# Kernel tuning notes

Hardware: AMD Instinct MI355X
Metric: run time of the kernel (lower is better)

Reference implementation:

```python
import jax, jax.numpy as jnp
import numpy as np

B, T, C = 4, 2048, 1024
H = 16
D = C // H          # 64 head dim
CS = 128            # chunk_size (hard-coded in module)


def setup_inputs() -> dict:
    key = jax.random.key(0)
    ks = jax.random.split(key, 6)
    scale = 0.02
    x = jax.random.normal(ks[0], (B, T, C), dtype=jnp.float32)
    Wq = jax.random.normal(ks[1], (C, C), dtype=jnp.float32) * scale
    Wk = jax.random.normal(ks[2], (C, C), dtype=jnp.float32) * scale
    Wv = jax.random.normal(ks[3], (C, C), dtype=jnp.float32) * scale
    Wo = jax.random.normal(ks[4], (C, C), dtype=jnp.float32) * scale
    alpha_raw = jnp.zeros((1, H, 1, 1), dtype=jnp.float32)
    beta_raw = jnp.zeros((1, H, 1, 1), dtype=jnp.float32)
    return {"x": x, "Wq": Wq, "Wk": Wk, "Wv": Wv, "Wo": Wo,
            "alpha_raw": alpha_raw, "beta_raw": beta_raw}


def reference(x, Wq, Wk, Wv, Wo, alpha_raw, beta_raw):
    Bb, Tt, Cc = x.shape
    nc = Tt // CS
    N = Bb * H * nc  # flattened (batch, head, chunk) recurrence lanes

    # projections -> [B, H, T, D]
    def proj(W):
        return (x @ W).reshape(Bb, Tt, H, D).transpose(0, 2, 1, 3)
    q, k, v = proj(Wq), proj(Wk), proj(Wv)
    # F.normalize(k, dim=-1) with eps=1e-12
    k = k / jnp.maximum(jnp.linalg.norm(k, axis=-1, keepdims=True), 1e-12)

    alpha = jax.nn.sigmoid(alpha_raw).reshape(H) * 0.5  # [H]
    beta = jax.nn.sigmoid(beta_raw).reshape(H) * 0.5    # [H]
    a = jnp.broadcast_to(alpha[None, :, None], (Bb, H, nc)).reshape(N, 1, 1)
    b = jnp.broadcast_to(beta[None, :, None], (Bb, H, nc)).reshape(N, 1, 1)

    # chunk layout [CS, N, D] for time-major scan
    def to_scan(u):
        return u.reshape(Bb, H, nc, CS, D).reshape(N, CS, D).transpose(1, 0, 2)
    qc, kc, vc = to_scan(q), to_scan(k), to_scan(v)

    # --- per-chunk operators: A = prod(I - a k k^T), B accumulates writes ---
    def op_step(carry, kv):
        A, Bo = carry
        kt, vt = kv  # [N, D]
        Ak = jnp.einsum('nij,nj->ni', A, kt)
        A = A - a * (Ak[:, :, None] * kt[:, None, :])
        Bk = jnp.einsum('nij,nj->ni', Bo, kt)
        Bo = Bo - a * (Bk[:, :, None] * kt[:, None, :]) + b * (vt[:, :, None] * kt[:, None, :])
        return (A, Bo), None

    A0 = jnp.broadcast_to(jnp.eye(D, dtype=x.dtype), (N, D, D))
    (Aop, Bop), _ = jax.lax.scan(op_step, (A0, jnp.zeros((N, D, D), x.dtype)), (kc, vc))

    # --- inter-chunk scan: M_{i+1} = M_i A_i + B_i ---
    Aop_c = Aop.reshape(Bb, H, nc, D, D).transpose(2, 0, 1, 3, 4)
    Bop_c = Bop.reshape(Bb, H, nc, D, D).transpose(2, 0, 1, 3, 4)

    def chunk_step(M, ab):
        Ai, Bi = ab
        return jnp.einsum('bhij,bhjk->bhik', M, Ai) + Bi, M

    M_final, M_starts = jax.lax.scan(
        chunk_step, jnp.zeros((Bb, H, D, D), x.dtype), (Aop_c, Bop_c))

    # --- intra-chunk application: y_t = M_t q_t; rank-1 delta update ---
    M0 = M_starts.transpose(1, 2, 0, 3, 4).reshape(N, D, D)

    def proc_step(M, qkv):
        qt, kt, vt = qkv
        yt = jnp.einsum('nij,nj->ni', M, qt)  # == q_t @ M^T (inference path)
        Mk = jnp.einsum('nij,nj->ni', M, kt)
        M = M - a * (Mk[:, :, None] * kt[:, None, :]) + b * (vt[:, :, None] * kt[:, None, :])
        return M, yt

    _, ys = jax.lax.scan(proc_step, M0, (qc, kc, vc))  # [CS, N, D]
    y = ys.transpose(1, 0, 2).reshape(Bb, H, Tt, D)
    y = y.transpose(0, 2, 1, 3).reshape(Bb, Tt, Cc)
    y = y @ Wo  # c_proj (dropout=0 -> identity)
    return (y, M_final)
```

## Files before the change

kernel.cpp:

```cpp
#include <hip/hip_runtime.h>
#include <stdint.h>


#define DEV __device__ __forceinline__

typedef __attribute__((ext_vector_type(4))) float f32x4;
typedef __attribute__((ext_vector_type(8))) __bf16 bf16x8;
typedef __attribute__((ext_vector_type(4))) __bf16 bf16x4;

typedef const __attribute__((address_space(1))) uint32_t* gas1_t;
typedef __attribute__((address_space(3))) uint32_t* las3_t;

DEV void gload_lds16(const void* g, void* l) {
  __builtin_amdgcn_global_load_lds((gas1_t)g, (las3_t)l, 16, 0, 0);
}

DEV float sgm(float x) { return 1.f / (1.f + __expf(-x)); }

template <int CTRL>
DEV float dpp_mov(float x) {
  return __builtin_bit_cast(
      float, __builtin_amdgcn_mov_dpp(__builtin_bit_cast(int, x), CTRL, 0xF, 0xF, true));
}
DEV float row16_reduce(float x) {
  x += dpp_mov<0x121>(x);
  x += dpp_mov<0x122>(x);
  x += dpp_mov<0x124>(x);
  x += dpp_mov<0x128>(x);
  return x;
}

DEV int swzb(int row, int col, int stride) {
  return ((row * stride + col) << 1) ^ ((row & 7) << 4);
}
DEV bf16x8 ldfrag(const __bf16* B, int row, int col, int stride) {
  return *(const bf16x8*)((const char*)B + swzb(row, col, stride));
}
DEV __bf16 ldsc(const __bf16* B, int row, int col, int stride) {
  return *(const __bf16*)((const char*)B + swzb(row, col, stride));
}
DEV void stb(__bf16* B, int row, int col, int stride, __bf16 v) {
  *(__bf16*)((char*)B + swzb(row, col, stride)) = v;
}
DEV void stb4(__bf16* B, int row, int c4, int stride, bf16x4 v) {
  *(bf16x4*)((char*)B + swzb(row, c4, stride)) = v;
}
DEV int goffn(int tr) {
  int m = tr >> 1;
  return (tr & 1) ? (2 * m * m + 4 * m + 2) : (2 * m * m + 2 * m);
}
DEV int stile(int tr, int sc) { return ((tr * (tr + 1)) / 2 + sc) * 256; }

__global__ __launch_bounds__(256) void cast_f32_bf16(const float* __restrict__ in,
                                                     __bf16* __restrict__ out) {
  int idx = blockIdx.x * 256 + threadIdx.x;
  float4 v = ((const float4*)in)[idx];
  bf16x4 o;
  o[0] = (__bf16)v.x; o[1] = (__bf16)v.y; o[2] = (__bf16)v.z; o[3] = (__bf16)v.w;
  ((bf16x4*)out)[idx] = o;
}

__global__ __launch_bounds__(256) void transpose_cast(const float* __restrict__ W,
                                                      __bf16* __restrict__ Wt) {
  __shared__ float tile[32][33];
  int tx = threadIdx.x & 31, ty = threadIdx.x >> 5;
  int n0 = blockIdx.x * 32, k0 = blockIdx.y * 32;
#pragma unroll
  for (int u = 0; u < 4; ++u)
    tile[ty + u * 8][tx] = W[(size_t)(k0 + ty + u * 8) * 1024 + n0 + tx];
  __syncthreads();
#pragma unroll
  for (int u = 0; u < 4; ++u)
    Wt[(size_t)(n0 + ty + u * 8) * 1024 + k0 + tx] = (__bf16)tile[tx][ty + u * 8];
}

template <int CALLS>
DEV void stage_tile(const __bf16* __restrict__ G, __bf16* L, int t, int wid, int K) {
#pragma unroll
  for (int it = 0; it < CALLS; ++it) {
    int e = it * 512 + t;
    int row = e >> 3;
    int c0 = ((e & 7) ^ (row & 7)) << 3;
    gload_lds16(G + (size_t)row * K + c0, L + it * 4096 + wid * 512);
  }
}

__global__ __launch_bounds__(512, 2) void gemm_bt(const __bf16* __restrict__ A,
                                                  const __bf16* __restrict__ Bt,
                                                  float* __restrict__ Cf,
                                                  __bf16* __restrict__ Cb,
                                                  int mode, int NBN) {
  const int t = threadIdx.x;
  const int wid = t >> 6, lane = t & 63;
  const int fr = lane & 15, fkq = lane >> 4, fk = fkq * 8;
  const int wr = wid >> 2, wc = wid & 3;
  const int K = 1024;
  int nwg = gridDim.x, lin = blockIdx.x;
  int q = nwg >> 3;
  int id2 = (lin & 7) * q + (lin >> 3);
  int bn = id2 % NBN, bm = id2 / NBN;
  __shared__ __bf16 lA[2][16384];
  __shared__ __bf16 lB[2][16384];
  const __bf16* Ab = A + (size_t)(bm * 256) * K;
  const __bf16* Bb = Bt + (size_t)(bn * 256) * K;
  f32x4 acc[8][4];
#pragma unroll
  for (int m = 0; m < 8; ++m)
#pragma unroll
    for (int nn = 0; nn < 4; ++nn) acc[m][nn] = 0.f;
  stage_tile<4>(Ab, lA[0], t, wid, K);
  stage_tile<4>(Bb, lB[0], t, wid, K);
  for (int kt = 0; kt < 16; ++kt) {
    int cur = kt & 1;
    asm volatile("s_barrier" ::: "memory");
    if (kt < 15) {
      stage_tile<4>(Ab + (kt + 1) * 64, lA[cur ^ 1], t, wid, K);
      stage_tile<4>(Bb + (kt + 1) * 64, lB[cur ^ 1], t, wid, K);
      asm volatile("s_waitcnt vmcnt(8)" ::: "memory");
    } else {
      asm volatile("s_waitcnt vmcnt(0)" ::: "memory");
    }
    asm volatile("s_barrier" ::: "memory");
#pragma unroll
    for (int kk = 0; kk < 2; ++kk) {
      bf16x8 bg[4];
#pragma unroll
      for (int nn = 0; nn < 4; ++nn)
        bg[nn] = ldfrag(lB[cur], wc * 64 + nn * 16 + fr, kk * 32 + fk, 64);
#pragma unroll
      for (int m = 0; m < 8; ++m) {
        bf16x8 af = ldfrag(lA[cur], wr * 128 + m * 16 + fr, kk * 32 + fk, 64);
#pragma unroll
        for (int nn = 0; nn < 4; ++nn)
          acc[m][nn] =
              __builtin_amdgcn_mfma_f32_16x16x32_bf16(af, bg[nn], acc[m][nn], 0, 0, 0);
      }
    }
  }
#pragma unroll
  for (int m = 0; m < 8; ++m) {
#pragma unroll
    for (int nn = 0; nn < 4; ++nn) {
#pragma unroll
      for (int rg = 0; rg < 4; ++rg) {
        int row = bm * 256 + wr * 128 + m * 16 + fkq * 4 + rg;
        int col = bn * 256 + wc * 64 + nn * 16 + fr;
        float val = acc[m][nn][rg];
        if (mode == 0) {
          Cf[(size_t)row * 1024 + col] = val;
        } else {
          int buf = col >> 10, cc = col & 1023;
          int b = row >> 11, tk = row & 2047;
          int h = cc >> 6, d = cc & 63;
          Cb[(size_t)buf * 8388608 + (((size_t)b * 16 + h) * 2048 + tk) * 64 + d] =
              (__bf16)val;
        }
      }
    }
  }
}

__global__ __launch_bounds__(512, 6) void wy_ab(const __bf16* __restrict__ kb,
                                                const __bf16* __restrict__ vb,
                                                const float* __restrict__ ar,
                                                const float* __restrict__ br,
                                                __bf16* __restrict__ Ug,
                                                __bf16* __restrict__ Wgb,
                                                __bf16* __restrict__ ATg,
                                                __bf16* __restrict__ Bop) {
  int n = blockIdx.x, h = (n >> 4) & 15;
  float a = sgm(ar[h]) * 0.5f;
  float b = sgm(br[h]) * 0.5f;
  int t = threadIdx.x, wid = t >> 6, lane = t & 63;
  int fr = lane & 15, fkq = lane >> 4, fk = fkq * 8;
  __shared__ __attribute__((aligned(16))) char pool[51200];
  __bf16* Ks  = (__bf16*)pool;
  __bf16* MTu = (__bf16*)pool;
  __bf16* MTw = (__bf16*)(pool + 16384);
  __bf16* Sng = (__bf16*)(pool + 32768);
  __bf16* KT  = (__bf16*)(pool + 32768);
  const __bf16* kg = kb + (size_t)n * 8192;
  const __bf16* vg = vb + (size_t)n * 8192;
  bf16x8 zz;
#pragma unroll
  for (int e = 0; e < 8; ++e) zz[e] = (__bf16)0.f;
  f32x4 c0 = {0.f, 0.f, 0.f, 0.f};
  bf16x4 kreg[4];
#pragma unroll
  for (int it = 0; it < 4; ++it) {
    int u = it * 512 + t;
    int row = u >> 4, c4 = (u & 15) * 4;
    bf16x4 kh = ((const bf16x4*)kg)[u];
    float kf[4];
#pragma unroll
    for (int e = 0; e < 4; ++e) kf[e] = (float)kh[e];
    float ssq = kf[0] * kf[0] + kf[1] * kf[1] + kf[2] * kf[2] + kf[3] * kf[3];
    ssq = row16_reduce(ssq);
    float inv = 1.f / fmaxf(sqrtf(ssq), 1e-12f);
    bf16x4 kn;
#pragma unroll
    for (int e = 0; e < 4; ++e) kn[e] = (__bf16)(kf[e] * inv);
    kreg[it] = kn;
    stb4(Ks, row, c4, 64, kn);
  }
  __syncthreads();
  for (int p = wid; p < 36; p += 8) {
    int tr = 0, pp = p;
    while (pp > tr) { pp -= (tr + 1); ++tr; }
    int sc = pp;
    f32x4 acc = {0.f, 0.f, 0.f, 0.f};
#pragma unroll
    for (int ks = 0; ks < 2; ++ks)
      acc = __builtin_amdgcn_mfma_f32_16x16x32_bf16(
          ldfrag(Ks, tr * 16 + fr, ks * 32 + fk, 64),
          ldfrag(Ks, sc * 16 + fr, ks * 32 + fk, 64), acc, 0, 0, 0);
    __bf16* dst = Sng + stile(tr, sc);
#pragma unroll
    for (int rg = 0; rg < 4; ++rg) {
      int r = fkq * 4 + rg;
      float v = -a * acc[rg];
      if (tr == sc && fr >= r) v = 0.f;
      dst[r * 16 + fr] = (__bf16)v;
    }
  }
  f32x4 U[4], W[4];
#pragma unroll
  for (int ct = 0; ct < 4; ++ct) {
#pragma unroll
    for (int rg = 0; rg < 4; ++rg) {
      int row = wid * 16 + fkq * 4 + rg, col = ct * 16 + fr;
      U[ct][rg] = (float)ldsc(Ks, row, col, 64);
      W[ct][rg] = b * (float)vg[row * 64 + col];
    }
  }
  __syncthreads();
  {
    __bf16* scr  = ((__bf16*)pool) + wid * 2048;
    __bf16* tNT  = scr;
    __bf16* tN2R = scr + 256;
    __bf16* tN2T = scr + 512;
    __bf16* tN4R = scr + 768;
    __bf16* tN4T = scr + 1024;
    __bf16* tN8T = scr + 1280;
    __bf16* tPR  = scr + 1536;
    __bf16* Nd = Sng + stile(wid, wid);
    float nv[4];
#pragma unroll
    for (int rg = 0; rg < 4; ++rg) {
      nv[rg] = (float)Nd[(fkq * 4 + rg) * 16 + fr];
      tNT[fr * 16 + fkq * 4 + rg] = (__bf16)nv[rg];
    }
    asm volatile("s_waitcnt lgkmcnt(0)" ::: "memory");
    bf16x8 af = (fk < 16) ? *(const bf16x8*)(Nd + fr * 16 + fk) : zz;
    bf16x8 bop = (fk < 16) ? *(const bf16x8*)(tNT + fr * 16 + fk) : zz;
    f32x4 X = __builtin_amdgcn_mfma_f32_16x16x32_bf16(af, bop, c0, 0, 0, 0);
#pragma unroll
    for (int rg = 0; rg < 4; ++rg) {
      __bf16 v = (__bf16)X[rg];
      tN2R[(fkq * 4 + rg) * 16 + fr] = v;
      tN2T[fr * 16 + fkq * 4 + rg] = v;
    }
    asm volatile("s_waitcnt lgkmcnt(0)" ::: "memory");
    af = (fk < 16) ? *(const bf16x8*)(tN2R + fr * 16 + fk) : zz;
    bop = (fk < 16) ? *(const bf16x8*)(tN2T + fr * 16 + fk) : zz;
    X = __builtin_amdgcn_mfma_f32_16x16x32_bf16(af, bop, c0, 0, 0, 0);
#pragma unroll
    for (int rg = 0; rg < 4; ++rg) {
      __bf16 v = (__bf16)X[rg];
      tN4R[(fkq * 4 + rg) * 16 + fr] = v;
      tN4T[fr * 16 + fkq * 4 + rg] = v;
    }
    asm volatile("s_waitcnt lgkmcnt(0)" ::: "memory");
    af = (fk < 16) ? *(const bf16x8*)(tN4R + fr * 16 + fk) : zz;
    bop = (fk < 16) ? *(const bf16x8*)(tN4T + fr * 16 + fk) : zz;
    X = __builtin_amdgcn_mfma_f32_16x16x32_bf16(af, bop, c0, 0, 0, 0);
#pragma unroll
    for (int rg = 0; rg < 4; ++rg)
      tN8T[fr * 16 + fkq * 4 + rg] = (__bf16)X[rg];
    f32x4 P;
#pragma unroll
    for (int rg = 0; rg < 4; ++rg)
      P[rg] = ((fkq * 4 + rg) == fr ? 1.f : 0.f) + nv[rg];
#pragma unroll
    for (int d = 0; d < 3; ++d) {
      const __bf16* tB = (d == 0) ? tN2T : (d == 1) ? tN4T : tN8T;
#pragma unroll
      for (int rg = 0; rg < 4; ++rg)
        tPR[(fkq * 4 + rg) * 16 + fr] = (__bf16)P[rg];
      asm volatile("s_waitcnt lgkmcnt(0)" ::: "memory");
      af = (fk < 16) ? *(const bf16x8*)(tPR + fr * 16 + fk) : zz;
      bop = (fk < 16) ? *(const bf16x8*)(tB + fr * 16 + fk) : zz;
      P = __builtin_amdgcn_mfma_f32_16x16x32_bf16(af, bop, P, 0, 0, 0);
    }
#pragma unroll
    for (int rg = 0; rg < 4; ++rg)
      Nd[(fkq * 4 + rg) * 16 + fr] = (__bf16)P[rg];
  }
  __syncthreads();
  for (int bb = 0; bb < 8; ++bb) {
    if (wid == bb) {
#pragma unroll
      for (int ct = 0; ct < 4; ++ct) {
        bf16x4 uu, ww;
#pragma unroll
        for (int rg = 0; rg < 4; ++rg) {
          uu[rg] = (__bf16)U[ct][rg];
          ww[rg] = (__bf16)W[ct][rg];
        }
        stb4(MTu, ct * 16 + fr, bb * 16 + fkq * 4, 128, uu);
        stb4(MTw, ct * 16 + fr, bb * 16 + fkq * 4, 128, ww);
      }
      asm volatile("s_waitcnt lgkmcnt(0)" ::: "memory");
      const __bf16* invT = Sng + stile(bb, bb);
      bf16x8 afv = (fk < 16) ? *(const bf16x8*)(invT + fr * 16 + fk) : zz;
#pragma unroll
      for (int ct = 0; ct < 4; ++ct) {
        bf16x8 bu = (fk < 16) ? ldfrag(MTu, ct * 16 + fr, bb * 16 + fk, 128) : zz;
        bf16x8 bw = (fk < 16) ? ldfrag(MTw, ct * 16 + fr, bb * 16 + fk, 128) : zz;
        U[ct] = __builtin_amdgcn_mfma_f32_16x16x32_bf16(afv, bu, c0, 0, 0, 0);
        W[ct] = __builtin_amdgcn_mfma_f32_16x16x32_bf16(afv, bw, c0, 0, 0, 0);
      }
#pragma unroll
      for (int ct = 0; ct < 4; ++ct) {
        bf16x4 uu, ww;
#pragma unroll
        for (int rg = 0; rg < 4; ++rg) {
          uu[rg] = (__bf16)U[ct][rg];
          ww[rg] = (__bf16)W[ct][rg];
        }
        stb4(MTu, ct * 16 + fr, bb * 16 + fkq * 4, 128, uu);
        stb4(MTw, ct * 16 + fr, bb * 16 + fkq * 4, 128, ww);
      }
    }
    __syncthreads();
    if (wid > bb) {
      bf16x8 af = zz;
      if (fk < 16) af = *(const bf16x8*)(Sng + stile(wid, bb) + fr * 16 + fk);
#pragma unroll
      for (int ct = 0; ct < 4; ++ct) {
        bf16x8 bu = zz, bw = zz;
        if (fk < 16) {
          bu = ldfrag(MTu, ct * 16 + fr, bb * 16 + fk, 128);
          bw = ldfrag(MTw, ct * 16 + fr, bb * 16 + fk, 128);
        }
        U[ct] = __builtin_amdgcn_mfma_f32_16x16x32_bf16(af, bu, U[ct], 0, 0, 0);
        W[ct] = __builtin_amdgcn_mfma_f32_16x16x32_bf16(af, bw, W[ct], 0, 0, 0);
      }
    }
  }
#pragma unroll
  for (int it = 0; it < 4; ++it) {
    int u = it * 512 + t;
    int row = u >> 4, c4 = (u & 15) * 4;
#pragma unroll
    for (int e = 0; e < 4; ++e) stb(KT, c4 + e, row, 128, kreg[it][e]);
  }
  __bf16* ugo = Ug + (size_t)n * 8192;
  __bf16* wgo = Wgb + (size_t)n * 8192;
#pragma unroll
  for (int ct = 0; ct < 4; ++ct)
#pragma unroll
    for (int rg = 0; rg < 4; ++rg) {
      int row = wid * 16 + fkq * 4 + rg, col = ct * 16 + fr;
      ugo[row * 64 + col] = (__bf16)U[ct][rg];
      wgo[row * 64 + col] = (__bf16)W[ct][rg];
    }
  __syncthreads();
#pragma unroll
  for (int q = 0; q < 4; ++q) {
    int tile = wid + q * 8;
    int mat = tile >> 4;
    int ti = (tile >> 2) & 3, tj = tile & 3;
    f32x4 acc = {0.f, 0.f, 0.f, 0.f};
    if (mat == 0) {
#pragma unroll
      for (int ks = 0; ks < 4; ++ks)
        acc = __builtin_amdgcn_mfma_f32_16x16x32_bf16(
            ldfrag(KT, ti * 16 + fr, ks * 32 + fk, 128),
            ldfrag(MTu, tj * 16 + fr, ks * 32 + fk, 128), acc, 0, 0, 0);
      char* dst = (char*)(ATg + (size_t)n * 4096);
#pragma unroll
      for (int rg = 0; rg < 4; ++rg) {
        int i = ti * 16 + fkq * 4 + rg, j = tj * 16 + fr;
        float v = (i == j ? 1.f : 0.f) - a * acc[rg];
        *(__bf16*)(dst + swzb(i, j, 64)) = (__bf16)v;
      }
    } else {
#pragma unroll
      for (int ks = 0; ks < 4; ++ks)
        acc = __builtin_amdgcn_mfma_f32_16x16x32_bf16(
            ldfrag(MTw, ti * 16 + fr, ks * 32 + fk, 128),
            ldfrag(KT, tj * 16 + fr, ks * 32 + fk, 128), acc, 0, 0, 0);
      __bf16* dst = Bop + (size_t)n * 4096;
#pragma unroll
      for (int rg = 0; rg < 4; ++rg)
        dst[(ti * 16 + fkq * 4 + rg) * 64 + tj * 16 + fr] = (__bf16)acc[rg];
    }
  }
}

__global__ __launch_bounds__(512) void chunk_scan(const __bf16* __restrict__ ATg,
                                                  const __bf16* __restrict__ Bop,
                                                  __bf16* __restrict__ Mst,
                                                  float* __restrict__ Mfinal) {
  int bh = blockIdx.x;
  int t = threadIdx.x, wid = t >> 6, lane = t & 63;
  int fr = lane & 15, fkq = lane >> 4, fk = fkq * 8;
  int ti = wid & 3, tj0 = (wid >> 2) << 1;
  __shared__ __bf16 Mh[4096];
  __shared__ __bf16 Ml[4096];
  __shared__ __bf16 At[2][4096];
  f32x4 acc[2];
  acc[0] = 0.f;
  acc[1] = 0.f;
  gload_lds16(ATg + (size_t)bh * 16 * 4096 + t * 8, At[0] + t * 8);
  for (int c = 0; c < 16; ++c) {
    int cur = c & 1;
    if (c < 15)
      gload_lds16(ATg + ((size_t)(bh * 16 + c + 1)) * 4096 + t * 8,
                  At[cur ^ 1] + t * 8);
    __bf16* mstc = Mst + ((size_t)(bh * 16 + c)) * 4096;
#pragma unroll
    for (int p = 0; p < 2; ++p) {
      int tj = tj0 + p;
#pragma unroll
      for (int rg = 0; rg < 4; ++rg) {
        int row = ti * 16 + fkq * 4 + rg, col = tj * 16 + fr;
        float v = acc[p][rg];
        __bf16 hi = (__bf16)v;
        mstc[row * 64 + col] = hi;
        stb(Mh, row, col, 64, hi);
        stb(Ml, row, col, 64, (__bf16)(v - (float)hi));
      }
    }
    __syncthreads();
    size_t bb = ((size_t)(bh * 16 + c)) * 4096;
#pragma unroll
    for (int p = 0; p < 2; ++p) {
      int tj = tj0 + p;
      f32x4 na;
#pragma unroll
      for (int rg = 0; rg < 4; ++rg)
        na[rg] = (float)Bop[bb + (ti * 16 + fkq * 4 + rg) * 64 + tj * 16 + fr];
#pragma unroll
      for (int ks = 0; ks < 2; ++ks) {
        bf16x8 bfrag = ldfrag(At[cur], tj * 16 + fr, ks * 32 + fk, 64);
        bf16x8 ah = ldfrag(Mh, ti * 16 + fr, ks * 32 + fk, 64);
        bf16x8 al = ldfrag(Ml, ti * 16 + fr, ks * 32 + fk, 64);
        na = __builtin_amdgcn_mfma_f32_16x16x32_bf16(ah, bfrag, na, 0, 0, 0);
        na = __builtin_amdgcn_mfma_f32_16x16x32_bf16(al, bfrag, na, 0, 0, 0);
      }
      acc[p] = na;
    }
    __syncthreads();
  }
#pragma unroll
  for (int p = 0; p < 2; ++p) {
    int tj = tj0 + p;
#pragma unroll
    for (int rg = 0; rg < 4; ++rg)
      Mfinal[(size_t)bh * 4096 + (ti * 16 + fkq * 4 + rg) * 64 + tj * 16 + fr] =
          acc[p][rg];
  }
}

__global__ __launch_bounds__(512, 4) void y_assemble(const __bf16* __restrict__ qb,
                                                     const __bf16* __restrict__ kb,
                                                     const __bf16* __restrict__ Ug,
                                                     const __bf16* __restrict__ Wgb,
                                                     const __bf16* __restrict__ Mst,
                                                     const float* __restrict__ ar,
                                                     __bf16* __restrict__ ybf) {
  int n = blockIdx.x, h = (n >> 4) & 15, b = n >> 8, c = n & 15;
  float a = sgm(ar[h]) * 0.5f;
  int t = threadIdx.x, wid = t >> 6, lane = t & 63;
  int fr = lane & 15, fk = (lane >> 4) * 8;
  __shared__ __bf16 Qs[8192];
  __shared__ __bf16 Rs[8192];
  __shared__ __bf16 M0s[4096];
  __shared__ __bf16 Gs[10240];
  __shared__ __bf16 WtT[8192];
  const __bf16* qg = qb + (size_t)n * 8192;
  const __bf16* kg = kb + (size_t)n * 8192;
  const __bf16* mg = Mst + (size_t)n * 4096;
#pragma unroll
  for (int it = 0; it < 4; ++it) {
    int u = it * 512 + t;
    int row = u >> 4, c4 = (u & 15) * 4;
    stb4(Qs, row, c4, 64, ((const bf16x4*)qg)[u]);
    bf16x4 kh = ((const bf16x4*)kg)[u];
    float kf[4];
#pragma unroll
    for (int e = 0; e < 4; ++e) kf[e] = (float)kh[e];
    float ssq = kf[0] * kf[0] + kf[1] * kf[1] + kf[2] * kf[2] + kf[3] * kf[3];
    ssq = row16_reduce(ssq);
    float inv = 1.f / fmaxf(sqrtf(ssq), 1e-12f);
    bf16x4 kn;
#pragma unroll
    for (int e = 0; e < 4; ++e) kn[e] = (__bf16)(kf[e] * inv);
    stb4(Rs, row, c4, 64, kn);
  }
#pragma unroll
  for (int it = 0; it < 2; ++it) {
    int u = it * 512 + t;
    int row = u >> 4, c4 = (u & 15) * 4;
    stb4(M0s, row, c4, 64, ((const bf16x4*)mg)[u]);
  }
#pragma unroll
  for (int pz = 0; pz < 2; ++pz) {
    int e = pz * 512 + t;
    int m = e >> 8, idx = e & 255;
    Gs[(2 * m * m + 4 * m + 1) * 256 + idx] = (__bf16)0.f;
  }
  __syncthreads();
  for (int p = wid; p < 36; p += 8) {
    int tr = 0, pp = p;
    while (pp > tr) { pp -= (tr + 1); ++tr; }
    int sc = pp;
    f32x4 acc = {0.f, 0.f, 0.f, 0.f};
#pragma unroll
    for (int ks = 0; ks < 2; ++ks)
      acc = __builtin_amdgcn_mfma_f32_16x16x32_bf16(
          ldfrag(Qs, tr * 16 + fr, ks * 32 + fk, 64),
          ldfrag(Rs, sc * 16 + fr, ks * 32 + fk, 64), acc, 0, 0, 0);
    int row0 = (lane >> 4) * 4, col = lane & 15;
    __bf16* gt = Gs + (goffn(tr) + sc) * 256;
#pragma unroll
    for (int rg = 0; rg < 4; ++rg) {
      int r = row0 + rg;
      float v = acc[rg];
      if (tr == sc && col >= r) v = 0.f;
      gt[r * 16 + col] = (__bf16)v;
    }
  }
  __syncthreads();
  const __bf16* ug = Ug + (size_t)n * 8192;
  const __bf16* wg = Wgb + (size_t)n * 8192;
#pragma unroll
  for (int it = 0; it < 4; ++it) {
    int u = it * 512 + t;
    int row = u >> 4, c4 = (u & 15) * 4;
    stb4(Rs, row, c4, 64, ((const bf16x4*)ug)[u]);
  }
  __syncthreads();
#pragma unroll
  for (int q = 0; q < 4; ++q) {
    int tile = wid + q * 8;
    int ti = tile >> 2, tj = tile & 3;
    f32x4 acc = {0.f, 0.f, 0.f, 0.f};
#pragma unroll
    for (int ks = 0; ks < 2; ++ks)
      acc = __builtin_amdgcn_mfma_f32_16x16x32_bf16(
          ldfrag(Rs, ti * 16 + fr, ks * 32 + fk, 64),
          ldfrag(M0s, tj * 16 + fr, ks * 32 + fk, 64), acc, 0, 0, 0);
    int row0 = (lane >> 4) * 4, col = lane & 15;
#pragma unroll
    for (int rg = 0; rg < 4; ++rg) {
      int s = ti * 16 + row0 + rg, i = tj * 16 + col;
      float wv = (float)wg[s * 64 + i];
      stb(WtT, i, s, 128, (__bf16)(wv - a * acc[rg]));
    }
  }
  __syncthreads();
  __bf16* yg = ybf + ((size_t)(b * 2048 + c * 128)) * 1024 + h * 64;
#pragma unroll
  for (int q = 0; q < 4; ++q) {
    int tile = wid + q * 8;
    int ti = tile >> 2, tj = tile & 3;
    f32x4 acc = {0.f, 0.f, 0.f, 0.f};
#pragma unroll
    for (int ks = 0; ks < 2; ++ks)
      acc = __builtin_amdgcn_mfma_f32_16x16x32_bf16(
          ldfrag(Qs, ti * 16 + fr, ks * 32 + fk, 64),
          ldfrag(M0s, tj * 16 + fr, ks * 32 + fk, 64), acc, 0, 0, 0);
    int goffv = goffn(ti);
    int np = (ti + 2) >> 1;
    for (int ks = 0; ks < np; ++ks) {
      int gtile = goffv + ks * 2 + (fk >> 4);
      bf16x8 af = *(const bf16x8*)(Gs + gtile * 256 + fr * 16 + (fk & 15));
      acc = __builtin_amdgcn_mfma_f32_16x16x32_bf16(
          af, ldfrag(WtT, tj * 16 + fr, ks * 32 + fk, 128), acc, 0, 0, 0);
    }
    int row0 = (lane >> 4) * 4, col = lane & 15;
#pragma unroll
    for (int rg = 0; rg < 4; ++rg) {
      int tt = ti * 16 + row0 + rg, d = tj * 16 + col;
      yg[(size_t)tt * 1024 + d] = (__bf16)acc[rg];
    }
  }
}

extern "C" void kernel_launch(void* const* d_in, const int* in_sizes, int n_in,
                              void* d_out, int out_size, void* d_ws, size_t ws_size,
                              hipStream_t stream) {
  const float* x  = (const float*)d_in[0];
  const float* Wq = (const float*)d_in[1];
  const float* Wk = (const float*)d_in[2];
  const float* Wv = (const float*)d_in[3];
  const float* Wo = (const float*)d_in[4];
  const float* ar = (const float*)d_in[5];
  const float* br = (const float*)d_in[6];

  char* ws = (char*)d_ws;
  __bf16* xb    = (__bf16*)ws;
  __bf16* ybf   = xb;
  __bf16* wqkvt = (__bf16*)(ws + (17u << 20));
  __bf16* wot   = (__bf16*)(ws + (23u << 20));
  __bf16* qb    = (__bf16*)(ws + (25u << 20));
  __bf16* kb    = qb + 8388608;
  __bf16* vb    = kb + 8388608;
  __bf16* Ugb   = (__bf16*)(ws + (76u << 20));
  __bf16* Wgb   = (__bf16*)(ws + (93u << 20));
  __bf16* ATg   = (__bf16*)(ws + (110u << 20));
  __bf16* Bop   = (__bf16*)(ws + (127u << 20));
  __bf16* Mst   = (__bf16*)(ws + (144u << 20));

  float* yout = (float*)d_out;
  float* Mfin = yout + 8388608;

  cast_f32_bf16<<<8192, 256, 0, stream>>>(x, xb);
  dim3 tg(32, 32);
  transpose_cast<<<tg, 256, 0, stream>>>(Wq, wqkvt);
  transpose_cast<<<tg, 256, 0, stream>>>(Wk, wqkvt + (1u << 20));
  transpose_cast<<<tg, 256, 0, stream>>>(Wv, wqkvt + (2u << 20));
  transpose_cast<<<tg, 256, 0, stream>>>(Wo, wot);

  gemm_bt<<<384, 512, 0, stream>>>(xb, wqkvt, nullptr, qb, 1, 12);

  wy_ab<<<1024, 512, 0, stream>>>(kb, vb, ar, br, Ugb, Wgb, ATg, Bop);
  chunk_scan<<<64, 512, 0, stream>>>(ATg, Bop, Mst, Mfin);
  y_assemble<<<1024, 512, 0, stream>>>(qb, kb, Ugb, Wgb, Mst, ar, ybf);

  gemm_bt<<<128, 512, 0, stream>>>(ybf, wot, yout, nullptr, 0, 4);
}
```

Baseline: 206.9 us.

## Shrink GEMM tiles to 128x128 with triple-buffered K=32 stages and merge weight transposes

The bf16 GEMM is retiled from 256x256 blocks of 512 threads to 128x128 blocks of 256 threads. It now uses a three-stage LDS ring over K=32 slices with a matching swizzle, and targets three blocks per CU. This raises the block count for both the QKV and output projections so the 256 CUs are better filled, at the cost of less operand reuse per block. The four weight transpose launches are also merged into one launch using a z-dimension, which cuts launch overhead.

```diff
diff --git a/kernel.cpp b/kernel.cpp
--- a/kernel.cpp
+++ b/kernel.cpp
@@ -60,8 +60,14 @@
   ((bf16x4*)out)[idx] = o;
 }
 
-__global__ __launch_bounds__(256) void transpose_cast(const float* __restrict__ W,
-                                                      __bf16* __restrict__ Wt) {
+__global__ __launch_bounds__(256) void transpose_cast4(const float* __restrict__ W0,
+                                                       const float* __restrict__ W1,
+                                                       const float* __restrict__ W2,
+                                                       const float* __restrict__ W3,
+                                                       __bf16* __restrict__ Wt) {
+  const float* W = (blockIdx.z == 0) ? W0 : (blockIdx.z == 1) ? W1
+                   : (blockIdx.z == 2) ? W2 : W3;
+  __bf16* dst = Wt + ((size_t)blockIdx.z << 20);
   __shared__ float tile[32][33];
   int tx = threadIdx.x & 31, ty = threadIdx.x >> 5;
   int n0 = blockIdx.x * 32, k0 = blockIdx.y * 32;
@@ -71,80 +77,86 @@
   __syncthreads();
 #pragma unroll
   for (int u = 0; u < 4; ++u)
-    Wt[(size_t)(n0 + ty + u * 8) * 1024 + k0 + tx] = (__bf16)tile[tx][ty + u * 8];
-}
-
-template <int CALLS>
-DEV void stage_tile(const __bf16* __restrict__ G, __bf16* L, int t, int wid, int K) {
-#pragma unroll
-  for (int it = 0; it < CALLS; ++it) {
-    int e = it * 512 + t;
-    int row = e >> 3;
-    int c0 = ((e & 7) ^ (row & 7)) << 3;
-    gload_lds16(G + (size_t)row * K + c0, L + it * 4096 + wid * 512);
-  }
-}
-
-__global__ __launch_bounds__(512, 2) void gemm_bt(const __bf16* __restrict__ A,
+    dst[(size_t)(n0 + ty + u * 8) * 1024 + k0 + tx] = (__bf16)tile[tx][ty + u * 8];
+}
+
+DEV void stage_tile32(const __bf16* __restrict__ G, __bf16* L, int t, int wid, int K) {
+#pragma unroll
+  for (int it = 0; it < 2; ++it) {
+    int e = it * 256 + t;
+    int row = e >> 2;
+    int c0 = ((e & 3) ^ (row & 3)) << 3;
+    gload_lds16(G + (size_t)row * K + c0, L + it * 2048 + wid * 512);
+  }
+}
+DEV bf16x8 ldfrag32(const __bf16* L, int row, int fkq) {
+  return *(const bf16x8*)(L + row * 32 + ((fkq ^ (row & 3)) << 3));
+}
+
+__global__ __launch_bounds__(256, 3) void gemm_bt(const __bf16* __restrict__ A,
                                                   const __bf16* __restrict__ Bt,
                                                   float* __restrict__ Cf,
                                                   __bf16* __restrict__ Cb,
                                                   int mode, int NBN) {
   const int t = threadIdx.x;
   const int wid = t >> 6, lane = t & 63;
-  const int fr = lane & 15, fkq = lane >> 4, fk = fkq * 8;
-  const int wr = wid >> 2, wc = wid & 3;
+  const int fr = lane & 15, fkq = lane >> 4;
+  const int wr = wid >> 1, wc = wid & 1;
   const int K = 1024;
   int nwg = gridDim.x, lin = blockIdx.x;
   int q = nwg >> 3;
   int id2 = (lin & 7) * q + (lin >> 3);
   int bn = id2 % NBN, bm = id2 / NBN;
-  __shared__ __bf16 lA[2][16384];
-  __shared__ __bf16 lB[2][16384];
-  const __bf16* Ab = A + (size_t)(bm * 256) * K;
-  const __bf16* Bb = Bt + (size_t)(bn * 256) * K;
-  f32x4 acc[8][4];
-#pragma unroll
-  for (int m = 0; m < 8; ++m)
+  __shared__ __bf16 lA[3][4096];
+  __shared__ __bf16 lB[3][4096];
+  const __bf16* Ab = A + (size_t)(bm * 128) * K;
+  const __bf16* Bb = Bt + (size_t)(bn * 128) * K;
+  f32x4 acc[4][4];
+#pragma unroll
+  for (int m = 0; m < 4; ++m)
 #pragma unroll
     for (int nn = 0; nn < 4; ++nn) acc[m][nn] = 0.f;
-  stage_tile<4>(Ab, lA[0], t, wid, K);
-  stage_tile<4>(Bb, lB[0], t, wid, K);
-  for (int kt = 0; kt < 16; ++kt) {
-    int cur = kt & 1;
+  stage_tile32(Ab, lA[0], t, wid, K);
+  stage_tile32(Bb, lB[0], t, wid, K);
+  stage_tile32(Ab + 32, lA[1], t, wid, K);
+  stage_tile32(Bb + 32, lB[1], t, wid, K);
+  int cur = 0;
+  for (int kt = 0; kt < 32; ++kt) {
     asm volatile("s_barrier" ::: "memory");
-    if (kt < 15) {
-      stage_tile<4>(Ab + (kt + 1) * 64, lA[cur ^ 1], t, wid, K);
-      stage_tile<4>(Bb + (kt + 1) * 64, lB[cur ^ 1], t, wid, K);
+    if (kt + 2 < 32) {
+      int nxt = cur >= 1 ? cur - 1 : cur + 2;
+      stage_tile32(Ab + (kt + 2) * 32, lA[nxt], t, wid, K);
+      stage_tile32(Bb + (kt + 2) * 32, lB[nxt], t, wid, K);
       asm volatile("s_waitcnt vmcnt(8)" ::: "memory");
+    } else if (kt + 1 < 32) {
+      asm volatile("s_waitcnt vmcnt(4)" ::: "memory");
     } else {
       asm volatile("s_waitcnt vmcnt(0)" ::: "memory");
     }
     asm volatile("s_barrier" ::: "memory");
-#pragma unroll
-    for (int kk = 0; kk < 2; ++kk) {
-      bf16x8 bg[4];
+    bf16x8 af[4], bg[4];
+#pragma unroll
+    for (int m = 0; m < 4; ++m)
+      af[m] = ldfrag32(lA[cur], wr * 64 + m * 16 + fr, fkq);
+#pragma unroll
+    for (int nn = 0; nn < 4; ++nn)
+      bg[nn] = ldfrag32(lB[cur], wc * 64 + nn * 16 + fr, fkq);
+#pragma unroll
+    for (int m = 0; m < 4; ++m)
 #pragma unroll
       for (int nn = 0; nn < 4; ++nn)
-        bg[nn] = ldfrag(lB[cur], wc * 64 + nn * 16 + fr, kk * 32 + fk, 64);
-#pragma unroll
-      for (int m = 0; m < 8; ++m) {
-        bf16x8 af = ldfrag(lA[cur], wr * 128 + m * 16 + fr, kk * 32 + fk, 64);
-#pragma unroll
-        for (int nn = 0; nn < 4; ++nn)
-          acc[m][nn] =
-              __builtin_amdgcn_mfma_f32_16x16x32_bf16(af, bg[nn], acc[m][nn], 0, 0, 0);
-      }
-    }
-  }
-#pragma unroll
-  for (int m = 0; m < 8; ++m) {
+        acc[m][nn] =
+            __builtin_amdgcn_mfma_f32_16x16x32_bf16(af[m], bg[nn], acc[m][nn], 0, 0, 0);
+    cur = (cur < 2) ? cur + 1 : 0;
+  }
+#pragma unroll
+  for (int m = 0; m < 4; ++m) {
 #pragma unroll
     for (int nn = 0; nn < 4; ++nn) {
 #pragma unroll
       for (int rg = 0; rg < 4; ++rg) {
-        int row = bm * 256 + wr * 128 + m * 16 + fkq * 4 + rg;
-        int col = bn * 256 + wc * 64 + nn * 16 + fr;
+        int row = bm * 128 + wr * 64 + m * 16 + fkq * 4 + rg;
+        int col = bn * 128 + wc * 64 + nn * 16 + fr;
         float val = acc[m][nn][rg];
         if (mode == 0) {
           Cf[(size_t)row * 1024 + col] = val;
@@ -605,7 +617,7 @@
   __bf16* xb    = (__bf16*)ws;
   __bf16* ybf   = xb;
   __bf16* wqkvt = (__bf16*)(ws + (17u << 20));
-  __bf16* wot   = (__bf16*)(ws + (23u << 20));
+  __bf16* wot   = wqkvt + (3u << 20);
   __bf16* qb    = (__bf16*)(ws + (25u << 20));
   __bf16* kb    = qb + 8388608;
   __bf16* vb    = kb + 8388608;
@@ -619,17 +631,13 @@
   float* Mfin = yout + 8388608;
 
   cast_f32_bf16<<<8192, 256, 0, stream>>>(x, xb);
-  dim3 tg(32, 32);
-  transpose_cast<<<tg, 256, 0, stream>>>(Wq, wqkvt);
-  transpose_cast<<<tg, 256, 0, stream>>>(Wk, wqkvt + (1u << 20));
-  transpose_cast<<<tg, 256, 0, stream>>>(Wv, wqkvt + (2u << 20));
-  transpose_cast<<<tg, 256, 0, stream>>>(Wo, wot);
-
-  gemm_bt<<<384, 512, 0, stream>>>(xb, wqkvt, nullptr, qb, 1, 12);
+  transpose_cast4<<<dim3(32, 32, 4), 256, 0, stream>>>(Wq, Wk, Wv, Wo, wqkvt);
+
+  gemm_bt<<<1536, 256, 0, stream>>>(xb, wqkvt, nullptr, qb, 1, 24);
 
   wy_ab<<<1024, 512, 0, stream>>>(kb, vb, ar, br, Ugb, Wgb, ATg, Bop);
   chunk_scan<<<64, 512, 0, stream>>>(ATg, Bop, Mst, Mfin);
   y_assemble<<<1024, 512, 0, stream>>>(qb, kb, Ugb, Wgb, Mst, ar, ybf);
 
-  gemm_bt<<<128, 512, 0, stream>>>(ybf, wot, yout, nullptr, 0, 4);
-}
+  gemm_bt<<<512, 256, 0, stream>>>(ybf, wot, yout, nullptr, 0, 8);
+}
```

Result: faster. 185.0 us (-10.6%).
